# Optimization experiments

Measured on AMD Instinct MI355X. Metric: run time of the kernel, lower is better.

The kernel has to match this reference:

```python
import jax, jax.numpy as jnp
from jax import lax
import numpy as np

DIM = 256
N_EMBED = 512
B = 16
T = 2048


def setup_inputs() -> dict:
    key = jax.random.key(0)
    k1, k2, k3 = jax.random.split(key, 3)
    inp = jax.random.normal(k1, (B, T, DIM), dtype=jnp.float32)
    spk = jax.random.normal(k2, (3, B, DIM), dtype=jnp.float32)
    embedding = jax.random.normal(k3, (N_EMBED, DIM, DIM), dtype=jnp.float32)
    return {"input": inp, "speaker_embedding": spk, "embedding": embedding}


def reference(input, speaker_embedding, embedding):
    x = input                              # (B, T, D)
    mul = speaker_embedding[2].T           # (D, B)
    add = speaker_embedding[1].T           # (D, B)
    # per-batch codebook: (n, D, D) @ (D, B) -> (n, D, B)
    cb = jnp.einsum('ndk,kb->ndb', embedding, mul)
    cb = cb / jnp.linalg.norm(cb, axis=1, keepdims=True)
    cb = cb + add                          # broadcast (D,B) over n
    embed = jnp.transpose(cb, (2, 1, 0))   # (B, D, n)
    # distances on detached values (matches torch .detach())
    flat = lax.stop_gradient(x)
    e = lax.stop_gradient(embed)
    dist = (jnp.sum(flat * flat, axis=2, keepdims=True)
            - 2.0 * jnp.einsum('btd,bdn->btn', flat, e)
            + jnp.sum(e * e, axis=1, keepdims=True))  # (B, T, n)
    embed_ind = jnp.argmax(-dist, axis=2)  # (B, T)
    cbB = jnp.transpose(cb, (2, 0, 1))     # (B, n, D)
    # per-batch gather of selected codes -> (B, T, D)
    quantize = cbB[jnp.arange(cbB.shape[0])[:, None], embed_ind]
    diff = jnp.mean((quantize - x) ** 2)
    quantize_1 = x + lax.stop_gradient(quantize - x)
    return ((quantize + quantize_1) / 2.0, diff, embed_ind)
```

## Files before the change

kernel.cpp:

```cpp
#include <hip/hip_runtime.h>

#define T_   2048
#define D_   256
#define N_   512
#define BTOT 16

typedef unsigned short ushortT;
typedef _Float16 f16;
typedef f16 h8 __attribute__((ext_vector_type(8)));
typedef float f4v __attribute__((ext_vector_type(4)));

#define QN   ((size_t)BTOT*T_*D_)
#define IDX0 (QN + 1)
#define CBSTRIDE ((size_t)N_*D_)

__device__ __forceinline__ float bf2f(ushortT u){
    union { unsigned int i; float f; } c; c.i = ((unsigned int)u) << 16; return c.f;
}
__device__ __forceinline__ void unp8(uint4 p, float* f){
    f[0]=bf2f((ushortT)(p.x & 0xffff)); f[1]=bf2f((ushortT)(p.x >> 16));
    f[2]=bf2f((ushortT)(p.y & 0xffff)); f[3]=bf2f((ushortT)(p.y >> 16));
    f[4]=bf2f((ushortT)(p.z & 0xffff)); f[5]=bf2f((ushortT)(p.z >> 16));
    f[6]=bf2f((ushortT)(p.w & 0xffff)); f[7]=bf2f((ushortT)(p.w >> 16));
}
__device__ __forceinline__ f4v mfma16(h8 a, h8 b, f4v c){
    return __builtin_amdgcn_mfma_f32_16x16x32_f16(a, b, c, 0, 0, 0);
}

__global__ void k_probe(const ushortT* __restrict__ x, int* __restrict__ flg){
    int tid = threadIdx.x;
    ushortT u = x[tid];
    int e = (u >> 7) & 0xff;
    bool ok = (e >= 100 && e <= 140);
    unsigned long long m = __ballot(ok);
    if (tid == 0) *flg = (__popcll(m) >= 55) ? 1 : 0;
}

__global__ __launch_bounds__(256) void k_codebook16(
    const void* __restrict__ spkin, const void* __restrict__ embin,
    f16* __restrict__ hig, f16* __restrict__ logp, float* __restrict__ e2g,
    f16* __restrict__ shi, f16* __restrict__ slo, float* __restrict__ se2,
    const int* __restrict__ flagp)
{
    const int isb = *flagp;
    const ushortT* ss = (const ushortT*)spkin;
    const float*   sf = (const float*)spkin;
    const ushortT* es = (const ushortT*)embin;
    const float*   ef = (const float*)embin;

    __shared__ float s2[D_ * 16];
    __shared__ float s1[D_ * 16];
    __shared__ float red[16 * D_];
    __shared__ float nrm[16];

    const int n = blockIdx.x, tid = threadIdx.x;

    for (int e = tid; e < D_ * 16; e += 256){
        int blc = e >> 8, k = e & 255;
        int g2 = (2*BTOT + blc)*D_ + k;
        int g1 = (1*BTOT + blc)*D_ + k;
        s2[k*16 + blc] = isb ? bf2f(ss[g2]) : sf[g2];
        s1[k*16 + blc] = isb ? bf2f(ss[g1]) : sf[g1];
    }
    __syncthreads();

    const int d = tid;
    float acc[16];
    #pragma unroll
    for (int b = 0; b < 16; b++) acc[b] = 0.f;

    const size_t rb = ((size_t)n * D_ + d) * D_;

    auto inner = [&](const float* ev, int k0){
        #pragma unroll
        for (int j = 0; j < 8; j++){
            float e = ev[j];
            const float4* sp = (const float4*)&s2[(k0 + j) * 16];
            float4 q0 = sp[0], q1 = sp[1], q2 = sp[2], q3 = sp[3];
            acc[0]  += e*q0.x; acc[1]  += e*q0.y; acc[2]  += e*q0.z; acc[3]  += e*q0.w;
            acc[4]  += e*q1.x; acc[5]  += e*q1.y; acc[6]  += e*q1.z; acc[7]  += e*q1.w;
            acc[8]  += e*q2.x; acc[9]  += e*q2.y; acc[10] += e*q2.z; acc[11] += e*q2.w;
            acc[12] += e*q3.x; acc[13] += e*q3.y; acc[14] += e*q3.z; acc[15] += e*q3.w;
        }
    };

    if (isb){
        for (int k0 = 0; k0 < D_; k0 += 8){
            uint4 p = *(const uint4*)(es + rb + k0);
            float ev[8]; unp8(p, ev);
            inner(ev, k0);
        }
    } else {
        for (int k0 = 0; k0 < D_; k0 += 8){
            float4 p0 = *(const float4*)(ef + rb + k0);
            float4 p1 = *(const float4*)(ef + rb + k0 + 4);
            float ev[8] = {p0.x,p0.y,p0.z,p0.w,p1.x,p1.y,p1.z,p1.w};
            inner(ev, k0);
        }
    }

    #pragma unroll
    for (int blc = 0; blc < 16; blc++) red[blc*D_ + d] = acc[blc]*acc[blc];
    __syncthreads();
    for (int s = 128; s > 0; s >>= 1){
        if (d < s){
            #pragma unroll
            for (int blc = 0; blc < 16; blc++) red[blc*D_ + d] += red[blc*D_ + d + s];
        }
        __syncthreads();
    }
    if (d < 16) nrm[d] = sqrtf(red[d*D_]);
    __syncthreads();

    float cbv[16];
    #pragma unroll
    for (int blc = 0; blc < 16; blc++)
        cbv[blc] = acc[blc] / nrm[blc] + s1[d*16 + blc];

    #pragma unroll
    for (int blc = 0; blc < 16; blc++) red[blc*D_ + d] = cbv[blc]*cbv[blc];
    __syncthreads();
    for (int s = 128; s > 0; s >>= 1){
        if (d < s){
            #pragma unroll
            for (int blc = 0; blc < 16; blc++) red[blc*D_ + d] += red[blc*D_ + d + s];
        }
        __syncthreads();
    }
    if (d < 16){
        float v = red[d*D_];
        if (d < 8) e2g[(size_t)d*N_ + n] = v;
        else       se2[(size_t)(d-8)*N_ + n] = v;
    }

    f16* sh = (f16*)s2;
    #pragma unroll
    for (int blc = 0; blc < 16; blc++){
        float c = cbv[blc];
        f16 h = (f16)c;
        float r = c - (float)h;
        f16 l = (f16)(r * 4096.f);
        sh[blc*256 + d] = h;
        sh[4096 + blc*256 + d] = l;
    }
    __syncthreads();
    for (int w = tid; w < 16*32; w += 256){
        const int blc = w >> 5, g = w & 31;
        const int d0 = (g>>2)*32 + (g&3)*8;
        const size_t off = (size_t)(blc & 7)*CBSTRIDE
                         + (size_t)((n>>4)*8 + (g>>2))*512
                         + (size_t)(g&3)*128 + (size_t)(n&15)*8;
        f16* dh = (blc < 8) ? hig  : shi;
        f16* dl = (blc < 8) ? logp : slo;
        *(uint4*)(dh + off) = *(const uint4*)(sh + blc*256 + d0);
        *(uint4*)(dl + off) = *(const uint4*)(sh + 4096 + blc*256 + d0);
    }
}

__global__ __launch_bounds__(256, 2) void k_fused(
    const void* __restrict__ xin,
    const f16* __restrict__ hig, const f16* __restrict__ logp,
    const float* __restrict__ e2g,
    float* __restrict__ outf, float* __restrict__ part,
    int blk0, const int* __restrict__ flagp)
{
    __shared__ float mv[4 * 16];
    __shared__ int   mi[4 * 16];
    __shared__ int   sfin[32];
    __shared__ float wsum[4];

    const int isb = *flagp;
    const int tid = threadIdx.x;
    const int bl = blockIdx.x & 7, tT = blockIdx.x >> 3;
    const int bg = blk0 + bl;
    const int lane = tid & 63, wid = tid >> 6;
    const int band = wid >> 1, nh = wid & 1;
    const int arow = lane & 15, kgrp = lane >> 4;

    const ushortT* xs = (const ushortT*)xin;
    const float*   xf = (const float*)xin;

    h8 ah[8], al[8];
    {
        const size_t rowbase = ((size_t)bg*T_ + (size_t)tT*32 + band*16 + arow) * D_;
        #pragma unroll
        for (int ks = 0; ks < 8; ks++){
            float f[8];
            const size_t o = rowbase + ks*32 + kgrp*8;
            if (isb){
                uint4 p = *(const uint4*)(xs + o);
                unp8(p, f);
            } else {
                float4 p0 = *(const float4*)(xf + o);
                float4 p1 = *(const float4*)(xf + o + 4);
                f[0]=p0.x; f[1]=p0.y; f[2]=p0.z; f[3]=p0.w;
                f[4]=p1.x; f[5]=p1.y; f[6]=p1.z; f[7]=p1.w;
            }
            h8 h, l;
            #pragma unroll
            for (int j = 0; j < 8; j++){
                f16 hh = (f16)f[j];
                h[j] = hh;
                l[j] = (f16)((f[j] - (float)hh) * 4096.f);
            }
            ah[ks] = h; al[ks] = l;
        }
    }

    const f16* hb = hig  + (size_t)bl*CBSTRIDE + (size_t)(lane*8);
    const f16* lb = logp + (size_t)bl*CBSTRIDE + (size_t)(lane*8);
    const float* e2b = e2g + (size_t)bl*N_;

    float runv[4]; int runi[4];
    #pragma unroll
    for (int i = 0; i < 4; i++){ runv[i] = 3.4e38f; runi[i] = 0x7fffffff; }

    h8 a0h, a1h, a0l, a1l;
    h8 b0h, b1h, b0l, b1l;

    const f16* hc = hb + (size_t)(nh*16)*4096;
    const f16* lc = lb + (size_t)(nh*16)*4096;

    a0h = *(const h8*)(hc);          a1h = *(const h8*)(hc + 4096);
    a0l = *(const h8*)(lc);          a1l = *(const h8*)(lc + 4096);

    f4v acch0, acch1, accm0, accm1, accl0, accl1;

    #pragma unroll 1
    for (int c = 0; c < 8; c++){
        acch0 = (f4v){0.f,0.f,0.f,0.f}; acch1 = acch0;
        accm0 = acch0; accm1 = acch0; accl0 = acch0; accl1 = acch0;

        #pragma unroll
        for (int ks2 = 0; ks2 < 4; ks2++){
            const int ks = ks2*2;
            {
                const f16* h2 = hc + (ks+1)*512;
                const f16* l2 = lc + (ks+1)*512;
                b0h = *(const h8*)(h2);       b1h = *(const h8*)(h2 + 4096);
                b0l = *(const h8*)(l2);       b1l = *(const h8*)(l2 + 4096);
            }
            acch0 = mfma16(ah[ks], a0h, acch0);
            acch1 = mfma16(ah[ks], a1h, acch1);
            accm0 = mfma16(ah[ks], a0l, accm0);
            accm1 = mfma16(ah[ks], a1l, accm1);
            accl0 = mfma16(al[ks], a0l, accl0);
            accl1 = mfma16(al[ks], a1l, accl1);
            accm0 = mfma16(al[ks], a0h, accm0);
            accm1 = mfma16(al[ks], a1h, accm1);
            if (ks2 < 3){
                const f16* h2 = hc + (ks+2)*512;
                const f16* l2 = lc + (ks+2)*512;
                a0h = *(const h8*)(h2);       a1h = *(const h8*)(h2 + 4096);
                a0l = *(const h8*)(l2);       a1l = *(const h8*)(l2 + 4096);
            } else if (c < 7){
                const f16* h2 = hc + 8192;
                const f16* l2 = lc + 8192;
                a0h = *(const h8*)(h2);       a1h = *(const h8*)(h2 + 4096);
                a0l = *(const h8*)(l2);       a1l = *(const h8*)(l2 + 4096);
            }
            acch0 = mfma16(ah[ks+1], b0h, acch0);
            acch1 = mfma16(ah[ks+1], b1h, acch1);
            accm0 = mfma16(ah[ks+1], b0l, accm0);
            accm1 = mfma16(ah[ks+1], b1l, accm1);
            accl0 = mfma16(al[ks+1], b0l, accl0);
            accl1 = mfma16(al[ks+1], b1l, accl1);
            accm0 = mfma16(al[ks+1], b0h, accm0);
            accm1 = mfma16(al[ks+1], b1h, accm1);
        }

        {
            const int nn0 = (nh*16 + c*2)*16 + arow;
            const float e20 = e2b[nn0], e21 = e2b[nn0 + 16];
            #pragma unroll
            for (int r = 0; r < 4; r++){
                float d0 = acch0[r] + accm0[r]*(1.f/4096.f) + accl0[r]*(1.f/16777216.f);
                float s0 = e20 - 2.f*d0;
                if (s0 < runv[r]){ runv[r] = s0; runi[r] = nn0; }
                float d1 = acch1[r] + accm1[r]*(1.f/4096.f) + accl1[r]*(1.f/16777216.f);
                float s1 = e21 - 2.f*d1;
                if (s1 < runv[r]){ runv[r] = s1; runi[r] = nn0 + 16; }
            }
        }
        hc += 8192; lc += 8192;
    }

    #pragma unroll
    for (int m = 8; m >= 1; m >>= 1){
        #pragma unroll
        for (int r = 0; r < 4; r++){
            float ov = __shfl_xor(runv[r], m);
            int   on = __shfl_xor(runi[r], m);
            if (ov < runv[r] || (ov == runv[r] && on < runi[r])){
                runv[r] = ov; runi[r] = on;
            }
        }
    }
    if (arow == 0){
        #pragma unroll
        for (int r = 0; r < 4; r++){
            mv[wid*16 + kgrp*4 + r] = runv[r];
            mi[wid*16 + kgrp*4 + r] = runi[r];
        }
    }
    __syncthreads();
    if (tid < 32){
        const int bandt = tid >> 4, rl = tid & 15;
        float v0 = mv[(bandt*2    )*16 + rl]; int i0 = mi[(bandt*2    )*16 + rl];
        float v1 = mv[(bandt*2 + 1)*16 + rl]; int i1 = mi[(bandt*2 + 1)*16 + rl];
        int nf = (v1 < v0) ? i1 : i0;
        sfin[tid] = nf;
        outf[IDX0 + (size_t)bg*T_ + (size_t)tT*32 + tid] = (float)nf;
    }
    __syncthreads();

    float dacc = 0.f;
    {
        const int r = tid >> 3, oct = tid & 7;
        const int nn = sfin[r];
        const size_t fb = (size_t)bl*CBSTRIDE
                        + (size_t)((nn>>4)*8 + oct)*512 + (size_t)(nn&15)*8;
        const size_t xo0 = ((size_t)bg*T_ + (size_t)tT*32 + r)*D_ + oct*32;
        #pragma unroll
        for (int q = 0; q < 4; q++){
            h8 hq = *(const h8*)(hig  + fb + q*128);
            h8 lq = *(const h8*)(logp + fb + q*128);
            float xv[8];
            if (isb){
                uint4 p = *(const uint4*)(xs + xo0 + q*8);
                unp8(p, xv);
            } else {
                float4 p0 = *(const float4*)(xf + xo0 + q*8);
                float4 p1 = *(const float4*)(xf + xo0 + q*8 + 4);
                xv[0]=p0.x; xv[1]=p0.y; xv[2]=p0.z; xv[3]=p0.w;
                xv[4]=p1.x; xv[5]=p1.y; xv[6]=p1.z; xv[7]=p1.w;
            }
            float og[8];
            #pragma unroll
            for (int j = 0; j < 8; j++){
                float qv = (float)hq[j] + (float)lq[j]*(1.f/4096.f);
                float qm = qv - xv[j];
                dacc += qm*qm;
                og[j] = 0.5f*(qv + (xv[j] + qm));
            }
            *(float4*)(outf + xo0 + q*8)     = make_float4(og[0],og[1],og[2],og[3]);
            *(float4*)(outf + xo0 + q*8 + 4) = make_float4(og[4],og[5],og[6],og[7]);
        }
    }
    #pragma unroll
    for (int o2 = 32; o2 > 0; o2 >>= 1) dacc += __shfl_down(dacc, o2, 64);
    if (lane == 0) wsum[wid] = dacc;
    __syncthreads();
    if (tid == 0){
        float t = wsum[0] + wsum[1] + wsum[2] + wsum[3];
        atomicAdd(&part[blockIdx.x & 1023], t);
    }
}

__global__ __launch_bounds__(256) void k_fin(const float* __restrict__ part,
                                             float* __restrict__ outf){
    const int tid = threadIdx.x;
    float v = part[tid] + part[tid + 256] + part[tid + 512] + part[tid + 768];
    #pragma unroll
    for (int o = 32; o > 0; o >>= 1) v += __shfl_down(v, o, 64);
    __shared__ float wsum[4];
    if ((tid & 63) == 0) wsum[tid >> 6] = v;
    __syncthreads();
    if (tid == 0)
        outf[QN] = (wsum[0] + wsum[1] + wsum[2] + wsum[3]) * (1.0f / (float)QN);
}

extern "C" void kernel_launch(void* const* d_in, const int* in_sizes, int n_in,
                              void* d_out, int out_size, void* d_ws, size_t ws_size,
                              hipStream_t stream)
{
    const void* x   = d_in[0];
    const void* spk = d_in[1];
    const void* emb = d_in[2];

    float* outf = (float*)d_out;

    char*  ws   = (char*)d_ws;
    f16*   hig  = (f16*)ws;
    f16*   logp = (f16*)(ws + (size_t)8*N_*D_*2);
    float* e2g  = (float*)(ws + (size_t)8*N_*D_*4);
    float* part = (float*)(ws + (size_t)8*N_*D_*4 + (size_t)8*N_*4);
    int*   flg  = (int*)((char*)part + 4096);

    f16*   shi = (f16*)outf;
    f16*   slo = (f16*)(outf + 524288);
    float* se2 = outf + 1048576;

    hipMemsetAsync(part, 0, 4096, stream);
    k_probe<<<1, 64, 0, stream>>>((const ushortT*)x, flg);

    k_codebook16<<<512, 256, 0, stream>>>(spk, emb, hig, logp, e2g,
                                          shi, slo, se2, flg);
    k_fused<<<512, 256, 0, stream>>>(x, shi, slo, se2, outf, part, 8, flg);
    k_fused<<<512, 256, 0, stream>>>(x, hig, logp, e2g, outf, part, 0, flg);
    k_fin<<<1, 256, 0, stream>>>(part, outf);
}
```

Measured before the change: 348.6 us.

## Stage codebook and input tiles through LDS, drop low-low MFMA term, enlarge blocks

The codebook kernel now loads embedding rows with coalesced loads into a swizzled LDS tile, prefetching the next chunk while it computes, instead of each thread reading its own strided row. The fused distance kernel uses 512-thread blocks covering 64 rows and stages x once in swizzled LDS for both the MFMA operand build and the output epilogue. It also prefetches B fragments through a 4-slot register ring and drops the low*low MFMA correction term. Dropping that term reduces precision in the distance computation, and the larger blocks use more LDS and fewer blocks per launch.

```diff
diff --git a/kernel.cpp b/kernel.cpp
--- a/kernel.cpp
+++ b/kernel.cpp
@@ -22,6 +22,10 @@
     f[2]=bf2f((ushortT)(p.y & 0xffff)); f[3]=bf2f((ushortT)(p.y >> 16));
     f[4]=bf2f((ushortT)(p.z & 0xffff)); f[5]=bf2f((ushortT)(p.z >> 16));
     f[6]=bf2f((ushortT)(p.w & 0xffff)); f[7]=bf2f((ushortT)(p.w >> 16));
+}
+__device__ __forceinline__ void unp4(uint2 p, float* f){
+    f[0]=bf2f((ushortT)(p.x & 0xffff)); f[1]=bf2f((ushortT)(p.x >> 16));
+    f[2]=bf2f((ushortT)(p.y & 0xffff)); f[3]=bf2f((ushortT)(p.y >> 16));
 }
 __device__ __forceinline__ f4v mfma16(h8 a, h8 b, f4v c){
     return __builtin_amdgcn_mfma_f32_16x16x32_f16(a, b, c, 0, 0, 0);
@@ -50,54 +54,90 @@
 
     __shared__ float s2[D_ * 16];
     __shared__ float s1[D_ * 16];
-    __shared__ float red[16 * D_];
+    __shared__ float tile[256 * 32];
     __shared__ float nrm[16];
+    float* red = tile;
 
     const int n = blockIdx.x, tid = threadIdx.x;
 
     for (int e = tid; e < D_ * 16; e += 256){
-        int blc = e >> 8, k = e & 255;
+        int k = e >> 4, blc = e & 15;
         int g2 = (2*BTOT + blc)*D_ + k;
         int g1 = (1*BTOT + blc)*D_ + k;
-        s2[k*16 + blc] = isb ? bf2f(ss[g2]) : sf[g2];
-        s1[k*16 + blc] = isb ? bf2f(ss[g1]) : sf[g1];
-    }
-    __syncthreads();
+        s2[e] = isb ? bf2f(ss[g2]) : sf[g2];
+        s1[e] = isb ? bf2f(ss[g1]) : sf[g1];
+    }
 
     const int d = tid;
     float acc[16];
     #pragma unroll
     for (int b = 0; b < 16; b++) acc[b] = 0.f;
 
-    const size_t rb = ((size_t)n * D_ + d) * D_;
-
-    auto inner = [&](const float* ev, int k0){
-        #pragma unroll
-        for (int j = 0; j < 8; j++){
-            float e = ev[j];
-            const float4* sp = (const float4*)&s2[(k0 + j) * 16];
-            float4 q0 = sp[0], q1 = sp[1], q2 = sp[2], q3 = sp[3];
-            acc[0]  += e*q0.x; acc[1]  += e*q0.y; acc[2]  += e*q0.z; acc[3]  += e*q0.w;
-            acc[4]  += e*q1.x; acc[5]  += e*q1.y; acc[6]  += e*q1.z; acc[7]  += e*q1.w;
-            acc[8]  += e*q2.x; acc[9]  += e*q2.y; acc[10] += e*q2.z; acc[11] += e*q2.w;
-            acc[12] += e*q3.x; acc[13] += e*q3.y; acc[14] += e*q3.z; acc[15] += e*q3.w;
+    float4 st[8];
+    uint4  st4[4];
+
+    const size_t embbase = (size_t)n * D_ * D_;
+
+    auto loadF = [&](int kc){
+        #pragma unroll
+        for (int r8 = 0; r8 < 8; r8++){
+            int row = r8*32 + (tid>>3);
+            st[r8] = *(const float4*)(ef + embbase + (size_t)row*D_ + kc + (tid&7)*4);
         }
     };
-
-    if (isb){
-        for (int k0 = 0; k0 < D_; k0 += 8){
-            uint4 p = *(const uint4*)(es + rb + k0);
-            float ev[8]; unp8(p, ev);
-            inner(ev, k0);
-        }
-    } else {
-        for (int k0 = 0; k0 < D_; k0 += 8){
-            float4 p0 = *(const float4*)(ef + rb + k0);
-            float4 p1 = *(const float4*)(ef + rb + k0 + 4);
-            float ev[8] = {p0.x,p0.y,p0.z,p0.w,p1.x,p1.y,p1.z,p1.w};
-            inner(ev, k0);
-        }
-    }
+    auto writeF = [&](){
+        #pragma unroll
+        for (int r8 = 0; r8 < 8; r8++){
+            int row = r8*32 + (tid>>3);
+            int idx = (row*32 + (tid&7)*4) ^ ((row&7)<<2);
+            *(float4*)&tile[idx] = st[r8];
+        }
+    };
+    auto loadB = [&](int kc){
+        #pragma unroll
+        for (int r4 = 0; r4 < 4; r4++){
+            int row = r4*64 + (tid>>2);
+            st4[r4] = *(const uint4*)(es + embbase + (size_t)row*D_ + kc + (tid&3)*8);
+        }
+    };
+    auto writeB = [&](){
+        #pragma unroll
+        for (int r4 = 0; r4 < 4; r4++){
+            int row = r4*64 + (tid>>2);
+            float f[8]; unp8(st4[r4], f);
+            int i0 = (row*32 + (tid&3)*8) ^ ((row&7)<<2);
+            int i1 = (row*32 + (tid&3)*8 + 4) ^ ((row&7)<<2);
+            *(float4*)&tile[i0] = make_float4(f[0],f[1],f[2],f[3]);
+            *(float4*)&tile[i1] = make_float4(f[4],f[5],f[6],f[7]);
+        }
+    };
+
+    if (isb) loadB(0); else loadF(0);
+
+    #pragma unroll 1
+    for (int c8 = 0; c8 < 8; c8++){
+        __syncthreads();
+        if (isb) writeB(); else writeF();
+        __syncthreads();
+        if (c8 < 7){ if (isb) loadB((c8+1)*32); else loadF((c8+1)*32); }
+        #pragma unroll
+        for (int j2 = 0; j2 < 8; j2++){
+            int idx = (d*32 + j2*4) ^ ((d&7)<<2);
+            float4 ev = *(const float4*)&tile[idx];
+            float evs[4] = {ev.x, ev.y, ev.z, ev.w};
+            #pragma unroll
+            for (int jj = 0; jj < 4; jj++){
+                float e = evs[jj];
+                const float4* sp = (const float4*)&s2[(c8*32 + j2*4 + jj) * 16];
+                float4 q0 = sp[0], q1 = sp[1], q2 = sp[2], q3 = sp[3];
+                acc[0]  += e*q0.x; acc[1]  += e*q0.y; acc[2]  += e*q0.z; acc[3]  += e*q0.w;
+                acc[4]  += e*q1.x; acc[5]  += e*q1.y; acc[6]  += e*q1.z; acc[7]  += e*q1.w;
+                acc[8]  += e*q2.x; acc[9]  += e*q2.y; acc[10] += e*q2.z; acc[11] += e*q2.w;
+                acc[12] += e*q3.x; acc[13] += e*q3.y; acc[14] += e*q3.z; acc[15] += e*q3.w;
+            }
+        }
+    }
+    __syncthreads();
 
     #pragma unroll
     for (int blc = 0; blc < 16; blc++) red[blc*D_ + d] = acc[blc]*acc[blc];
@@ -157,17 +197,27 @@
     }
 }
 
-__global__ __launch_bounds__(256, 2) void k_fused(
+#define ISSUE(cc, kss, slot) do{                                   \
+    const f16* hc_ = hb + (size_t)(cc)*8192;                       \
+    const f16* lc_ = lb + (size_t)(cc)*8192;                       \
+    bh0[slot] = *(const h8*)(hc_ + (kss)*512);                     \
+    bh1[slot] = *(const h8*)(hc_ + 4096 + (kss)*512);              \
+    bl0[slot] = *(const h8*)(lc_ + (kss)*512);                     \
+    bl1[slot] = *(const h8*)(lc_ + 4096 + (kss)*512);              \
+}while(0)
+
+__global__ __launch_bounds__(512, 2) void k_fused(
     const void* __restrict__ xin,
     const f16* __restrict__ hig, const f16* __restrict__ logp,
     const float* __restrict__ e2g,
     float* __restrict__ outf, float* __restrict__ part,
     int blk0, const int* __restrict__ flagp)
 {
-    __shared__ float mv[4 * 16];
-    __shared__ int   mi[4 * 16];
-    __shared__ int   sfin[32];
-    __shared__ float wsum[4];
+    __shared__ float xt[64 * 256];
+    __shared__ float mv[8 * 16];
+    __shared__ int   mi[8 * 16];
+    __shared__ int   sfin[64];
+    __shared__ float wsum[8];
 
     const int isb = *flagp;
     const int tid = threadIdx.x;
@@ -177,25 +227,46 @@
     const int band = wid >> 1, nh = wid & 1;
     const int arow = lane & 15, kgrp = lane >> 4;
 
-    const ushortT* xs = (const ushortT*)xin;
-    const float*   xf = (const float*)xin;
+    const f16* hb = hig  + (size_t)bl*CBSTRIDE + (size_t)(nh*16)*4096 + (size_t)lane*8;
+    const f16* lb = logp + (size_t)bl*CBSTRIDE + (size_t)(nh*16)*4096 + (size_t)lane*8;
+    const float* e2b = e2g + (size_t)bl*N_;
+
+    h8 bh0[4], bh1[4], bl0[4], bl1[4];
+    ISSUE(0, 0, 0); ISSUE(0, 1, 1); ISSUE(0, 2, 2);
+
+    const size_t xrow0 = (size_t)bg*T_ + (size_t)tT*64;
+    if (isb){
+        const ushortT* xs = (const ushortT*)xin;
+        #pragma unroll
+        for (int it = 0; it < 8; it++){
+            int r = it*8 + wid;
+            uint2 p = *(const uint2*)(xs + (xrow0 + r)*D_ + lane*4);
+            float f[4]; unp4(p, f);
+            int idx = (r*256 + lane*4) ^ ((r&7)<<2);
+            *(float4*)&xt[idx] = make_float4(f[0],f[1],f[2],f[3]);
+        }
+    } else {
+        const float* xf = (const float*)xin;
+        #pragma unroll
+        for (int it = 0; it < 8; it++){
+            int r = it*8 + wid;
+            float4 p = *(const float4*)(xf + (xrow0 + r)*D_ + lane*4);
+            int idx = (r*256 + lane*4) ^ ((r&7)<<2);
+            *(float4*)&xt[idx] = p;
+        }
+    }
+    __syncthreads();
 
     h8 ah[8], al[8];
     {
-        const size_t rowbase = ((size_t)bg*T_ + (size_t)tT*32 + band*16 + arow) * D_;
+        const int rr = band*16 + arow;
+        const int sw = (rr&7)<<2;
         #pragma unroll
         for (int ks = 0; ks < 8; ks++){
-            float f[8];
-            const size_t o = rowbase + ks*32 + kgrp*8;
-            if (isb){
-                uint4 p = *(const uint4*)(xs + o);
-                unp8(p, f);
-            } else {
-                float4 p0 = *(const float4*)(xf + o);
-                float4 p1 = *(const float4*)(xf + o + 4);
-                f[0]=p0.x; f[1]=p0.y; f[2]=p0.z; f[3]=p0.w;
-                f[4]=p1.x; f[5]=p1.y; f[6]=p1.z; f[7]=p1.w;
-            }
+            int base = rr*256 + ks*32 + kgrp*8;
+            float4 f0 = *(const float4*)&xt[(base    ) ^ sw];
+            float4 f1 = *(const float4*)&xt[(base + 4) ^ sw];
+            float f[8] = {f0.x,f0.y,f0.z,f0.w,f1.x,f1.y,f1.z,f1.w};
             h8 h, l;
             #pragma unroll
             for (int j = 0; j < 8; j++){
@@ -207,82 +278,33 @@
         }
     }
 
-    const f16* hb = hig  + (size_t)bl*CBSTRIDE + (size_t)(lane*8);
-    const f16* lb = logp + (size_t)bl*CBSTRIDE + (size_t)(lane*8);
-    const float* e2b = e2g + (size_t)bl*N_;
-
     float runv[4]; int runi[4];
     #pragma unroll
     for (int i = 0; i < 4; i++){ runv[i] = 3.4e38f; runi[i] = 0x7fffffff; }
-
-    h8 a0h, a1h, a0l, a1l;
-    h8 b0h, b1h, b0l, b1l;
-
-    const f16* hc = hb + (size_t)(nh*16)*4096;
-    const f16* lc = lb + (size_t)(nh*16)*4096;
-
-    a0h = *(const h8*)(hc);          a1h = *(const h8*)(hc + 4096);
-    a0l = *(const h8*)(lc);          a1l = *(const h8*)(lc + 4096);
-
-    f4v acch0, acch1, accm0, accm1, accl0, accl1;
 
     #pragma unroll 1
     for (int c = 0; c < 8; c++){
-        acch0 = (f4v){0.f,0.f,0.f,0.f}; acch1 = acch0;
-        accm0 = acch0; accm1 = acch0; accl0 = acch0; accl1 = acch0;
-
-        #pragma unroll
-        for (int ks2 = 0; ks2 < 4; ks2++){
-            const int ks = ks2*2;
-            {
-                const f16* h2 = hc + (ks+1)*512;
-                const f16* l2 = lc + (ks+1)*512;
-                b0h = *(const h8*)(h2);       b1h = *(const h8*)(h2 + 4096);
-                b0l = *(const h8*)(l2);       b1l = *(const h8*)(l2 + 4096);
-            }
-            acch0 = mfma16(ah[ks], a0h, acch0);
-            acch1 = mfma16(ah[ks], a1h, acch1);
-            accm0 = mfma16(ah[ks], a0l, accm0);
-            accm1 = mfma16(ah[ks], a1l, accm1);
-            accl0 = mfma16(al[ks], a0l, accl0);
-            accl1 = mfma16(al[ks], a1l, accl1);
-            accm0 = mfma16(al[ks], a0h, accm0);
-            accm1 = mfma16(al[ks], a1h, accm1);
-            if (ks2 < 3){
-                const f16* h2 = hc + (ks+2)*512;
-                const f16* l2 = lc + (ks+2)*512;
-                a0h = *(const h8*)(h2);       a1h = *(const h8*)(h2 + 4096);
-                a0l = *(const h8*)(l2);       a1l = *(const h8*)(l2 + 4096);
-            } else if (c < 7){
-                const f16* h2 = hc + 8192;
-                const f16* l2 = lc + 8192;
-                a0h = *(const h8*)(h2);       a1h = *(const h8*)(h2 + 4096);
-                a0l = *(const h8*)(l2);       a1l = *(const h8*)(l2 + 4096);
-            }
-            acch0 = mfma16(ah[ks+1], b0h, acch0);
-            acch1 = mfma16(ah[ks+1], b1h, acch1);
-            accm0 = mfma16(ah[ks+1], b0l, accm0);
-            accm1 = mfma16(ah[ks+1], b1l, accm1);
-            accl0 = mfma16(al[ks+1], b0l, accl0);
-            accl1 = mfma16(al[ks+1], b1l, accl1);
-            accm0 = mfma16(al[ks+1], b0h, accm0);
-            accm1 = mfma16(al[ks+1], b1h, accm1);
-        }
-
-        {
-            const int nn0 = (nh*16 + c*2)*16 + arow;
-            const float e20 = e2b[nn0], e21 = e2b[nn0 + 16];
-            #pragma unroll
-            for (int r = 0; r < 4; r++){
-                float d0 = acch0[r] + accm0[r]*(1.f/4096.f) + accl0[r]*(1.f/16777216.f);
-                float s0 = e20 - 2.f*d0;
-                if (s0 < runv[r]){ runv[r] = s0; runi[r] = nn0; }
-                float d1 = acch1[r] + accm1[r]*(1.f/4096.f) + accl1[r]*(1.f/16777216.f);
-                float s1 = e21 - 2.f*d1;
-                if (s1 < runv[r]){ runv[r] = s1; runi[r] = nn0 + 16; }
-            }
-        }
-        hc += 8192; lc += 8192;
+        f4v a0 = (f4v){0.f,0.f,0.f,0.f}, a1 = a0, m0 = a0, m1 = a0;
+        #pragma unroll
+        for (int ks = 0; ks < 8; ks++){
+            if (ks < 5)      { ISSUE(c,   ks+3, (ks+3)&3); }
+            else if (c < 7)  { ISSUE(c+1, ks-5, (ks+3)&3); }
+            a0 = mfma16(ah[ks], bh0[ks&3], a0);
+            a1 = mfma16(ah[ks], bh1[ks&3], a1);
+            m0 = mfma16(ah[ks], bl0[ks&3], m0);
+            m1 = mfma16(ah[ks], bl1[ks&3], m1);
+            m0 = mfma16(al[ks], bh0[ks&3], m0);
+            m1 = mfma16(al[ks], bh1[ks&3], m1);
+        }
+        const int nn0 = (nh*16 + c*2)*16 + arow;
+        const float e20 = e2b[nn0], e21 = e2b[nn0 + 16];
+        #pragma unroll
+        for (int r = 0; r < 4; r++){
+            float s0 = e20 - 2.f*(a0[r] + m0[r]*(1.f/4096.f));
+            if (s0 < runv[r]){ runv[r] = s0; runi[r] = nn0; }
+            float s1 = e21 - 2.f*(a1[r] + m1[r]*(1.f/4096.f));
+            if (s1 < runv[r]){ runv[r] = s1; runi[r] = nn0 + 16; }
+        }
     }
 
     #pragma unroll
@@ -304,37 +326,32 @@
         }
     }
     __syncthreads();
-    if (tid < 32){
+    if (tid < 64){
         const int bandt = tid >> 4, rl = tid & 15;
         float v0 = mv[(bandt*2    )*16 + rl]; int i0 = mi[(bandt*2    )*16 + rl];
         float v1 = mv[(bandt*2 + 1)*16 + rl]; int i1 = mi[(bandt*2 + 1)*16 + rl];
         int nf = (v1 < v0) ? i1 : i0;
         sfin[tid] = nf;
-        outf[IDX0 + (size_t)bg*T_ + (size_t)tT*32 + tid] = (float)nf;
+        outf[IDX0 + (size_t)bg*T_ + (size_t)tT*64 + tid] = (float)nf;
     }
     __syncthreads();
 
     float dacc = 0.f;
     {
         const int r = tid >> 3, oct = tid & 7;
+        const int sw = (r&7)<<2;
         const int nn = sfin[r];
         const size_t fb = (size_t)bl*CBSTRIDE
                         + (size_t)((nn>>4)*8 + oct)*512 + (size_t)(nn&15)*8;
-        const size_t xo0 = ((size_t)bg*T_ + (size_t)tT*32 + r)*D_ + oct*32;
+        const size_t xo0 = ((size_t)bg*T_ + (size_t)tT*64 + r)*D_ + oct*32;
         #pragma unroll
         for (int q = 0; q < 4; q++){
             h8 hq = *(const h8*)(hig  + fb + q*128);
             h8 lq = *(const h8*)(logp + fb + q*128);
-            float xv[8];
-            if (isb){
-                uint4 p = *(const uint4*)(xs + xo0 + q*8);
-                unp8(p, xv);
-            } else {
-                float4 p0 = *(const float4*)(xf + xo0 + q*8);
-                float4 p1 = *(const float4*)(xf + xo0 + q*8 + 4);
-                xv[0]=p0.x; xv[1]=p0.y; xv[2]=p0.z; xv[3]=p0.w;
-                xv[4]=p1.x; xv[5]=p1.y; xv[6]=p1.z; xv[7]=p1.w;
-            }
+            int xb = r*256 + oct*32 + q*8;
+            float4 x0 = *(const float4*)&xt[(xb    ) ^ sw];
+            float4 x1 = *(const float4*)&xt[(xb + 4) ^ sw];
+            float xv[8] = {x0.x,x0.y,x0.z,x0.w,x1.x,x1.y,x1.z,x1.w};
             float og[8];
             #pragma unroll
             for (int j = 0; j < 8; j++){
@@ -352,10 +369,13 @@
     if (lane == 0) wsum[wid] = dacc;
     __syncthreads();
     if (tid == 0){
-        float t = wsum[0] + wsum[1] + wsum[2] + wsum[3];
+        float t = 0.f;
+        #pragma unroll
+        for (int i = 0; i < 8; i++) t += wsum[i];
         atomicAdd(&part[blockIdx.x & 1023], t);
     }
 }
+#undef ISSUE
 
 __global__ __launch_bounds__(256) void k_fin(const float* __restrict__ part,
                                              float* __restrict__ outf){
@@ -396,7 +416,7 @@
 
     k_codebook16<<<512, 256, 0, stream>>>(spk, emb, hig, logp, e2g,
                                           shi, slo, se2, flg);
-    k_fused<<<512, 256, 0, stream>>>(x, shi, slo, se2, outf, part, 8, flg);
-    k_fused<<<512, 256, 0, stream>>>(x, hig, logp, e2g, outf, part, 0, flg);
+    k_fused<<<256, 512, 0, stream>>>(x, shi, slo, se2, outf, part, 8, flg);
+    k_fused<<<256, 512, 0, stream>>>(x, hig, logp, e2g, outf, part, 0, flg);
     k_fin<<<1, 256, 0, stream>>>(part, outf);
 }
```

Result: faster. 333.9 us (-4.2%).
